# Kernel optimization log

Measured on AMD Instinct MI355X. Metric: run time of the kernel, lower is better.

## Reference

```python
import jax, jax.numpy as jnp
import numpy as np

EPS = 1e-6

def setup_inputs() -> dict:
    key = jax.random.key(0)
    ks = jax.random.split(key, 9)
    B, D, F = 8192, 2048, 1024
    s_in = 1.0 / np.sqrt(D)
    return {
        "Q": jax.random.normal(ks[0], (B, D), jnp.float32),
        "K": jax.random.normal(ks[1], (B, D), jnp.float32),
        "V": jax.random.normal(ks[2], (B, D), jnp.float32),
        "Wq": jax.random.normal(ks[3], (D, F), jnp.float32) * s_in,
        "bq": jnp.zeros((F,), jnp.float32),
        "Wk": jax.random.normal(ks[4], (D, F), jnp.float32) * s_in,
        "bk": jnp.zeros((F,), jnp.float32),
        "Wv": jax.random.normal(ks[5], (D, D), jnp.float32) * s_in,
        "bv": jnp.zeros((D,), jnp.float32),
    }

def reference(Q, K, V, Wq, bq, Wk, bk, Wv, bv):
    # feature maps: Linear + ELU (note: ELU, no +1, matching the source)
    Q_feat = jax.nn.elu(Q @ Wq + bq)          # (B, F)
    K_feat = jax.nn.elu(K @ Wk + bk)          # (B, F)
    V_proj = V @ Wv + bv                      # (B, D)
    # torch: KV = outer(K_feat, V_proj); QKV = Q_feat @ KV
    # equivalent without materializing (B, F, D):
    qk = jnp.einsum('bi,bi->b', Q_feat, K_feat)      # (B,)
    QKV = qk[:, None] * V_proj                        # (B, D)
    # Z = 1 / (sum_i Q_feat * sum_i K_feat + eps)
    Z = 1.0 / (Q_feat.sum(-1) * K_feat.sum(-1) + EPS)  # (B,)
    return QKV * Z[:, None]
```

## Files before the change

### kernel.cpp

```cpp
#include <hip/hip_runtime.h>
#include <hip/hip_fp16.h>
#include <cstdint>
#include <cstddef>

typedef _Float16 f16x8 __attribute__((ext_vector_type(8)));
typedef _Float16 f16x4 __attribute__((ext_vector_type(4)));
typedef float    f32x4 __attribute__((ext_vector_type(4)));

#define GPTR(p) ((const __attribute__((address_space(1))) void*)(p))
#define SPTR(p) ((__attribute__((address_space(3))) void*)(p))

__global__ void transpose_cast_kernel(const float* __restrict__ W,
                                      _Float16* __restrict__ Wt,
                                      int R, int C) {
  __shared__ float tile[32][33];
  const int c  = blockIdx.x * 32 + threadIdx.x;
  const int r0 = blockIdx.y * 32;
  for (int i = threadIdx.y; i < 32; i += 8)
    tile[i][threadIdx.x] = W[(size_t)(r0 + i) * C + c];
  __syncthreads();
  const int out_c = r0 + threadIdx.x;
  const int oc0   = blockIdx.x * 32;
  for (int i = threadIdx.y; i < 32; i += 8)
    Wt[(size_t)(oc0 + i) * R + out_c] = (_Float16)tile[threadIdx.x][i];
}

__global__ void cast_f32_f16_kernel(const float* __restrict__ src,
                                    _Float16* __restrict__ dst) {
  const size_t i = (size_t)blockIdx.x * 256 + threadIdx.x;
  const float4 v = ((const float4*)src)[i];
  f16x4 h;
  h[0] = (_Float16)v.x; h[1] = (_Float16)v.y;
  h[2] = (_Float16)v.z; h[3] = (_Float16)v.w;
  ((f16x4*)dst)[i] = h;
}

#define STG8(kk, h, slotv) do {                                                \
    __builtin_amdgcn_global_load_lds(GPTR(aRow + (h) * hstep + (kk)),          \
        SPTR(Aring + (slotv) * 4096 + wave * 512), 16, 0, 0);                  \
    __builtin_amdgcn_global_load_lds(GPTR(bRow + (h) * hstep + (kk)),          \
        SPTR(Bring + (slotv) * 4096 + wave * 512), 16, 0, 0);                  \
  } while (0)

#define WINDOW8(t_, DOSTG, VCSTR) do {                                         \
    const int e_ = (2 * (t_)) & 7;                                             \
    if (DOSTG) STG8(((t_) + 3) * 32, 0, (e_ + 6) & 7);                         \
    asm volatile("s_waitcnt vmcnt(" VCSTR ")" ::: "memory");                   \
    __builtin_amdgcn_s_barrier();                                              \
    asm volatile("" ::: "memory");                                             \
    const _Float16* Ab_ = Aring + ((e_ + wm) & 7) * 4096;                      \
    const _Float16* Bb_ = Bring + ((e_ + (wn >> 1)) & 7) * 4096               \
                          + (wn & 1) * 2048;                                   \
    f16x8 bf_[4], af_[4];                                                      \
    _Pragma("unroll")                                                          \
    for (int j_ = 0; j_ < 4; ++j_)                                             \
      bf_[j_] = *(const f16x8*)(Bb_ + j_ * 512 + lane_c * 8);                  \
    _Pragma("unroll")                                                          \
    for (int i_ = 0; i_ < 4; ++i_)                                             \
      af_[i_] = *(const f16x8*)(Ab_ + i_ * 512 + lane_c * 8);                  \
    __builtin_amdgcn_s_setprio(1);                                             \
    _Pragma("unroll")                                                          \
    for (int i_ = 0; i_ < 4; ++i_)                                             \
      _Pragma("unroll")                                                        \
      for (int j_ = 0; j_ < 4; ++j_)                                           \
        acc[i_][j_] = __builtin_amdgcn_mfma_f32_16x16x32_f16(af_[i_], bf_[j_], \
                                                             acc[i_][j_],      \
                                                             0, 0, 0);         \
    __builtin_amdgcn_s_setprio(0);                                             \
    asm volatile("" ::: "memory");                                             \
    __builtin_amdgcn_s_barrier();                                              \
    if (DOSTG) STG8(((t_) + 3) * 32, 1, (e_ + 7) & 7);                         \
    __builtin_amdgcn_s_barrier();                                              \
    asm volatile("" ::: "memory");                                             \
    _Pragma("unroll")                                                          \
    for (int i_ = 0; i_ < 4; ++i_)                                             \
      af_[i_] = *(const f16x8*)(Ab_ + (i_ + 4) * 512 + lane_c * 8);            \
    __builtin_amdgcn_s_setprio(1);                                             \
    _Pragma("unroll")                                                          \
    for (int i_ = 0; i_ < 4; ++i_)                                             \
      _Pragma("unroll")                                                        \
      for (int j_ = 0; j_ < 4; ++j_)                                           \
        acc[i_ + 4][j_] = __builtin_amdgcn_mfma_f32_16x16x32_f16(af_[i_],      \
                                                                 bf_[j_],      \
                                                                 acc[i_ + 4][j_],\
                                                                 0, 0, 0);     \
    __builtin_amdgcn_s_setprio(0);                                             \
    asm volatile("" ::: "memory");                                             \
    __builtin_amdgcn_s_barrier();                                              \
  } while (0)

template <int MODE, bool OUTHALF>
__global__ __launch_bounds__(512, 2) void gemm8p(
    const _Float16* __restrict__ A,
    const _Float16* __restrict__ Bt0, const _Float16* __restrict__ Bt1,
    const float* __restrict__ bias0, const float* __restrict__ bias1,
    int msplit, const float* __restrict__ scale,
    void* __restrict__ Cv, int K, int N) {
  __shared__ __align__(16) _Float16 Aring[8 * 4096];
  __shared__ __align__(16) _Float16 Bring[8 * 4096];

  const int tid  = threadIdx.x;
  const int lane = tid & 63;
  const int wave = tid >> 6;
  const int quad = lane >> 4;
  const int r    = lane & 15;
  const int wm   = wave >> 2;
  const int wn   = wave & 3;

  const int gx  = gridDim.x;
  const int nwg = gx * gridDim.y;
  int flat = blockIdx.y * gx + blockIdx.x;
  if ((nwg & 7) == 0) flat = (flat & 7) * (nwg >> 3) + (flat >> 3);
  const int m0 = (flat / gx) * 256;
  const int n0 = (flat % gx) * 256;

  const _Float16* Bt   = (m0 >= msplit) ? Bt1 : Bt0;
  const float*    bias = (m0 >= msplit) ? bias1 : bias0;

  const int sp  = tid >> 3;
  const int sub = (tid & 7) ^ (sp & 7);
  const int lr  = sp * 2 + (sub >> 2);
  const int sc  = sub & 3;
  const _Float16* aRow = A  + (size_t)(m0 + lr) * K + sc * 8;
  const _Float16* bRow = Bt + (size_t)(n0 + lr) * K + sc * 8;
  const int hstep = 128 * K;

  const int lane_c = (r >> 1) * 8 + (((((r & 1) << 2) | quad)) ^ (r >> 1));

  f32x4 acc[8][4] = {};
  const int NT = K >> 5;

#pragma unroll
  for (int tt = 0; tt < 3; ++tt) {
    STG8(tt * 32, 0, (2 * tt) & 7);
    STG8(tt * 32, 1, (2 * tt + 1) & 7);
  }

  for (int t = 0; t < NT - 3; ++t) WINDOW8(t, 1, "10");
  WINDOW8(NT - 3, 0, "8");
  WINDOW8(NT - 2, 0, "4");
  WINDOW8(NT - 1, 0, "0");

  float*    Cf = (float*)Cv;
  _Float16* Ch = (_Float16*)Cv;
#pragma unroll
  for (int i = 0; i < 8; ++i) {
    const int row0 = m0 + wm * 128 + i * 16 + quad * 4;
#pragma unroll
    for (int j = 0; j < 4; ++j) {
      const int col = n0 + wn * 64 + j * 16 + r;
      const float b = bias[col];
#pragma unroll
      for (int reg = 0; reg < 4; ++reg) {
        const int row = row0 + reg;
        float v = acc[i][j][reg] + b;
        if (MODE == 0) v = v > 0.f ? v : (expf(v) - 1.f);
        else           v = v * scale[row];
        if (OUTHALF) Ch[(size_t)row * N + col] = (_Float16)v;
        else         Cf[(size_t)row * N + col] = v;
      }
    }
  }
}

#undef STG8
#undef WINDOW8

template <int MODE, bool AHALF, bool OUTHALF>
__global__ __launch_bounds__(256) void gemm2(
    const void* __restrict__ Av,
    const _Float16* __restrict__ Bt0, const _Float16* __restrict__ Bt1,
    const float* __restrict__ bias0, const float* __restrict__ bias1,
    int msplit, const float* __restrict__ scale,
    void* __restrict__ Cv, int K, int N) {
  constexpr int BK = 64;
  __shared__ __align__(16) _Float16 As[128 * BK];
  __shared__ __align__(16) _Float16 Bs[128 * BK];

  const int tid  = threadIdx.x;
  const int lane = tid & 63;
  const int wave = tid >> 6;
  const int quad = lane >> 4;
  const int r    = lane & 15;
  const int wm   = wave >> 1;
  const int wn   = wave & 1;
  const int m0   = blockIdx.y * 128;
  const int n0   = blockIdx.x * 128;

  const _Float16* Bt  = (m0 >= msplit) ? Bt1 : Bt0;
  const float* bias   = (m0 >= msplit) ? bias1 : bias0;

  size_t aoff[4], boff[4];
  int slot[4];
#pragma unroll
  for (int t = 0; t < 4; ++t) {
    const int s  = wave * 256 + t * 64 + lane;
    const int n  = s >> 3;
    const int kc = (s & 7) ^ (n & 7);
    aoff[t] = (size_t)(m0 + n) * K + kc * 8;
    boff[t] = (size_t)(n0 + n) * K + kc * 8;
    slot[t] = s;
  }

  f32x4 acc[4][4] = {};
  const _Float16* Ah = (const _Float16*)Av;
  const float*    Af = (const float*)Av;

  for (int k0 = 0; k0 < K; k0 += BK) {
    __syncthreads();
    if (AHALF) {
#pragma unroll
      for (int t = 0; t < 4; ++t)
        __builtin_amdgcn_global_load_lds(GPTR(Ah + aoff[t] + k0),
                                         SPTR(As + (wave * 256 + t * 64) * 8),
                                         16, 0, 0);
    } else {
#pragma unroll
      for (int t = 0; t < 4; ++t) {
        const float* ap = Af + aoff[t] + k0;
        const float4 v0 = *(const float4*)ap;
        const float4 v1 = *(const float4*)(ap + 4);
        f16x8 h;
        h[0] = (_Float16)v0.x; h[1] = (_Float16)v0.y;
        h[2] = (_Float16)v0.z; h[3] = (_Float16)v0.w;
        h[4] = (_Float16)v1.x; h[5] = (_Float16)v1.y;
        h[6] = (_Float16)v1.z; h[7] = (_Float16)v1.w;
        *(f16x8*)(As + (size_t)slot[t] * 8) = h;
      }
    }
#pragma unroll
    for (int t = 0; t < 4; ++t)
      __builtin_amdgcn_global_load_lds(GPTR(Bt + boff[t] + k0),
                                       SPTR(Bs + (wave * 256 + t * 64) * 8),
                                       16, 0, 0);
    __syncthreads();

#pragma unroll
    for (int ki = 0; ki < 2; ++ki) {
      f16x8 af[4], bf[4];
#pragma unroll
      for (int i = 0; i < 4; ++i) {
        const int an = wm * 64 + i * 16 + r;
        af[i] = *(const f16x8*)(As + (an * 8 + ((ki * 4 + quad) ^ (an & 7))) * 8);
      }
#pragma unroll
      for (int j = 0; j < 4; ++j) {
        const int bn = wn * 64 + j * 16 + r;
        bf[j] = *(const f16x8*)(Bs + (bn * 8 + ((ki * 4 + quad) ^ (bn & 7))) * 8);
      }
#pragma unroll
      for (int i = 0; i < 4; ++i)
#pragma unroll
        for (int j = 0; j < 4; ++j)
          acc[i][j] = __builtin_amdgcn_mfma_f32_16x16x32_f16(af[i], bf[j],
                                                             acc[i][j], 0, 0, 0);
    }
  }

  float*    Cf = (float*)Cv;
  _Float16* Ch = (_Float16*)Cv;
#pragma unroll
  for (int i = 0; i < 4; ++i) {
#pragma unroll
    for (int j = 0; j < 4; ++j) {
      const int col = n0 + wn * 64 + j * 16 + r;
      const float b = bias[col];
#pragma unroll
      for (int reg = 0; reg < 4; ++reg) {
        const int row = m0 + wm * 64 + i * 16 + quad * 4 + reg;
        float v = acc[i][j][reg] + b;
        if (MODE == 0) v = v > 0.f ? v : (expf(v) - 1.f);
        else           v = v * scale[row];
        if (OUTHALF) Ch[(size_t)row * N + col] = (_Float16)v;
        else         Cf[(size_t)row * N + col] = v;
      }
    }
  }
}

template <bool HALF>
__global__ void reduce_scale2(const void* __restrict__ Qf,
                              const void* __restrict__ Kf,
                              float* __restrict__ scale) {
  const int b = blockIdx.x;
  const int t = threadIdx.x;
  float q[4], k[4];
  if (HALF) {
    const f16x4 qh = ((const f16x4*)((const _Float16*)Qf + (size_t)b * 1024))[t];
    const f16x4 kh = ((const f16x4*)((const _Float16*)Kf + (size_t)b * 1024))[t];
#pragma unroll
    for (int i = 0; i < 4; ++i) { q[i] = (float)qh[i]; k[i] = (float)kh[i]; }
  } else {
    const float4 qv = ((const float4*)((const float*)Qf + (size_t)b * 1024))[t];
    const float4 kv = ((const float4*)((const float*)Kf + (size_t)b * 1024))[t];
    q[0] = qv.x; q[1] = qv.y; q[2] = qv.z; q[3] = qv.w;
    k[0] = kv.x; k[1] = kv.y; k[2] = kv.z; k[3] = kv.w;
  }
  float qk = q[0] * k[0] + q[1] * k[1] + q[2] * k[2] + q[3] * k[3];
  float sq = q[0] + q[1] + q[2] + q[3];
  float sk = k[0] + k[1] + k[2] + k[3];
#pragma unroll
  for (int off = 32; off > 0; off >>= 1) {
    qk += __shfl_down(qk, off, 64);
    sq += __shfl_down(sq, off, 64);
    sk += __shfl_down(sk, off, 64);
  }
  __shared__ float buf[3][4];
  const int lane = t & 63, wv = t >> 6;
  if (lane == 0) { buf[0][wv] = qk; buf[1][wv] = sq; buf[2][wv] = sk; }
  __syncthreads();
  if (t == 0) {
    const float QK = buf[0][0] + buf[0][1] + buf[0][2] + buf[0][3];
    const float SQ = buf[1][0] + buf[1][1] + buf[1][2] + buf[1][3];
    const float SK = buf[2][0] + buf[2][1] + buf[2][2] + buf[2][3];
    scale[b] = QK / (SQ * SK + 1e-6f);
  }
}

extern "C" void kernel_launch(void* const* d_in, const int* in_sizes, int n_in,
                              void* d_out, int out_size, void* d_ws,
                              size_t ws_size, hipStream_t stream) {
  const float* Q  = (const float*)d_in[0];
  const float* K_ = (const float*)d_in[1];
  const float* V  = (const float*)d_in[2];
  const float* Wq = (const float*)d_in[3];
  const float* bq = (const float*)d_in[4];
  const float* Wk = (const float*)d_in[5];
  const float* bk = (const float*)d_in[6];
  const float* Wv = (const float*)d_in[7];
  const float* bv = (const float*)d_in[8];
  float* out = (float*)d_out;

  const int B = 8192, D = 2048, F = 1024;
  const size_t MiB = 1u << 20;
  char* ws = (char*)d_ws;

  const size_t NEED_FAST = 40 * MiB + 64 * 1024;

  if (ws_size >= NEED_FAST) {
    _Float16* WqT = (_Float16*)ws;
    _Float16* WkT = (_Float16*)(ws + 4 * MiB);
    _Float16* WvT = (_Float16*)ws;
    _Float16* QfH = (_Float16*)(ws + 8 * MiB);
    _Float16* KfH = (_Float16*)(ws + 24 * MiB);
    _Float16* Vh  = (_Float16*)(ws + 8 * MiB);
    float* scale  = (float*)(ws + 40 * MiB);
    _Float16* Qh = (_Float16*)d_out;
    _Float16* Kh = (_Float16*)d_out + (size_t)B * D;

    dim3 tb(32, 8);
    transpose_cast_kernel<<<dim3(F / 32, D / 32), tb, 0, stream>>>(Wq, WqT, D, F);
    transpose_cast_kernel<<<dim3(F / 32, D / 32), tb, 0, stream>>>(Wk, WkT, D, F);
    const int castBlocks = (B * D / 4) / 256;
    cast_f32_f16_kernel<<<castBlocks, 256, 0, stream>>>(Q,  Qh);
    cast_f32_f16_kernel<<<castBlocks, 256, 0, stream>>>(K_, Kh);

    gemm8p<0, true><<<dim3(F / 256, (2 * B) / 256), 512, 0, stream>>>(
        Qh, WqT, WkT, bq, bk, B, nullptr, QfH, D, F);
    reduce_scale2<true><<<B, 256, 0, stream>>>(QfH, KfH, scale);

    cast_f32_f16_kernel<<<castBlocks, 256, 0, stream>>>(V, Vh);
    transpose_cast_kernel<<<dim3(D / 32, D / 32), tb, 0, stream>>>(Wv, WvT, D, D);
    gemm8p<1, false><<<dim3(D / 256, B / 256), 512, 0, stream>>>(
        Vh, WvT, WvT, bv, bv, 1 << 30, scale, out, D, D);
  } else {
    _Float16* WqT = (_Float16*)ws;
    _Float16* WkT = (_Float16*)(ws + 4 * MiB);
    _Float16* WvT = (_Float16*)(ws + 8 * MiB);
    float* scale  = (float*)(ws + 16 * MiB);
    float* Qf = out;
    float* Kf = out + (size_t)B * F;

    dim3 tb(32, 8);
    transpose_cast_kernel<<<dim3(F / 32, D / 32), tb, 0, stream>>>(Wq, WqT, D, F);
    transpose_cast_kernel<<<dim3(F / 32, D / 32), tb, 0, stream>>>(Wk, WkT, D, F);
    transpose_cast_kernel<<<dim3(D / 32, D / 32), tb, 0, stream>>>(Wv, WvT, D, D);

    gemm2<0, false, false><<<dim3(F / 128, B / 128), 256, 0, stream>>>(
        Q, WqT, WqT, bq, bq, 1 << 30, nullptr, Qf, D, F);
    gemm2<0, false, false><<<dim3(F / 128, B / 128), 256, 0, stream>>>(
        K_, WkT, WkT, bk, bk, 1 << 30, nullptr, Kf, D, F);
    reduce_scale2<false><<<B, 256, 0, stream>>>(Qf, Kf, scale);
    gemm2<1, false, false><<<dim3(D / 128, B / 128), 256, 0, stream>>>(
        V, WvT, WvT, bv, bv, 1 << 30, scale, out, D, D);
  }
}
```

Baseline: 441.1 us.

## Collapse GEMM K-window to a single barrier and issue prefetch mid-MFMA

```diff
diff --git a/kernel.cpp b/kernel.cpp
--- a/kernel.cpp
+++ b/kernel.cpp
@@ -42,51 +42,45 @@
         SPTR(Bring + (slotv) * 4096 + wave * 512), 16, 0, 0);                  \
   } while (0)
 
-#define WINDOW8(t_, DOSTG, VCSTR) do {                                         \
+#define WINDOW8(t_, DOSTG, DOWAIT, VCSTR) do {                                 \
     const int e_ = (2 * (t_)) & 7;                                             \
-    if (DOSTG) STG8(((t_) + 3) * 32, 0, (e_ + 6) & 7);                         \
-    asm volatile("s_waitcnt vmcnt(" VCSTR ")" ::: "memory");                   \
-    __builtin_amdgcn_s_barrier();                                              \
-    asm volatile("" ::: "memory");                                             \
     const _Float16* Ab_ = Aring + ((e_ + wm) & 7) * 4096;                      \
-    const _Float16* Bb_ = Bring + ((e_ + (wn >> 1)) & 7) * 4096               \
+    const _Float16* Bb_ = Bring + ((e_ + (wn >> 1)) & 7) * 4096                \
                           + (wn & 1) * 2048;                                   \
-    f16x8 bf_[4], af_[4];                                                      \
+    f16x8 bf_[4], afL_[4], afH_[4];                                            \
     _Pragma("unroll")                                                          \
     for (int j_ = 0; j_ < 4; ++j_)                                             \
       bf_[j_] = *(const f16x8*)(Bb_ + j_ * 512 + lane_c * 8);                  \
     _Pragma("unroll")                                                          \
     for (int i_ = 0; i_ < 4; ++i_)                                             \
-      af_[i_] = *(const f16x8*)(Ab_ + i_ * 512 + lane_c * 8);                  \
+      afL_[i_] = *(const f16x8*)(Ab_ + i_ * 512 + lane_c * 8);                 \
+    _Pragma("unroll")                                                          \
+    for (int i_ = 0; i_ < 4; ++i_)                                             \
+      afH_[i_] = *(const f16x8*)(Ab_ + (i_ + 4) * 512 + lane_c * 8);           \
     __builtin_amdgcn_s_setprio(1);                                             \
     _Pragma("unroll")                                                          \
     for (int i_ = 0; i_ < 4; ++i_)                                             \
       _Pragma("unroll")                                                        \
       for (int j_ = 0; j_ < 4; ++j_)                                           \
-        acc[i_][j_] = __builtin_amdgcn_mfma_f32_16x16x32_f16(af_[i_], bf_[j_], \
+        acc[i_][j_] = __builtin_amdgcn_mfma_f32_16x16x32_f16(afL_[i_], bf_[j_],\
                                                              acc[i_][j_],      \
                                                              0, 0, 0);         \
-    __builtin_amdgcn_s_setprio(0);                                             \
-    asm volatile("" ::: "memory");                                             \
-    __builtin_amdgcn_s_barrier();                                              \
-    if (DOSTG) STG8(((t_) + 3) * 32, 1, (e_ + 7) & 7);                         \
-    __builtin_amdgcn_s_barrier();                                              \
-    asm volatile("" ::: "memory");                                             \
-    _Pragma("unroll")                                                          \
-    for (int i_ = 0; i_ < 4; ++i_)                                             \
-      af_[i_] = *(const f16x8*)(Ab_ + (i_ + 4) * 512 + lane_c * 8);            \
-    __builtin_amdgcn_s_setprio(1);                                             \
+    if (DOSTG) {                                                               \
+      STG8(((t_) + 3) * 32, 0, (e_ + 6) & 7);                                  \
+      STG8(((t_) + 3) * 32, 1, (e_ + 7) & 7);                                  \
+    }                                                                          \
     _Pragma("unroll")                                                          \
     for (int i_ = 0; i_ < 4; ++i_)                                             \
       _Pragma("unroll")                                                        \
       for (int j_ = 0; j_ < 4; ++j_)                                           \
-        acc[i_ + 4][j_] = __builtin_amdgcn_mfma_f32_16x16x32_f16(af_[i_],      \
+        acc[i_ + 4][j_] = __builtin_amdgcn_mfma_f32_16x16x32_f16(afH_[i_],     \
                                                                  bf_[j_],      \
                                                                  acc[i_ + 4][j_],\
                                                                  0, 0, 0);     \
     __builtin_amdgcn_s_setprio(0);                                             \
+    if (DOWAIT) asm volatile("s_waitcnt vmcnt(" VCSTR ")" ::: "memory");       \
+    __builtin_amdgcn_s_barrier();                                              \
     asm volatile("" ::: "memory");                                             \
-    __builtin_amdgcn_s_barrier();                                              \
   } while (0)
 
 template <int MODE, bool OUTHALF>
@@ -135,11 +129,14 @@
     STG8(tt * 32, 0, (2 * tt) & 7);
     STG8(tt * 32, 1, (2 * tt + 1) & 7);
   }
-
-  for (int t = 0; t < NT - 3; ++t) WINDOW8(t, 1, "10");
-  WINDOW8(NT - 3, 0, "8");
-  WINDOW8(NT - 2, 0, "4");
-  WINDOW8(NT - 1, 0, "0");
+  asm volatile("s_waitcnt vmcnt(8)" ::: "memory");
+  __builtin_amdgcn_s_barrier();
+  asm volatile("" ::: "memory");
+
+  for (int t = 0; t < NT - 3; ++t) WINDOW8(t, 1, 1, "8");
+  WINDOW8(NT - 3, 0, 1, "4");
+  WINDOW8(NT - 2, 0, 1, "0");
+  WINDOW8(NT - 1, 0, 0, "0");
 
   float*    Cf = (float*)Cv;
   _Float16* Ch = (_Float16*)Cv;
```

New measurement: 394.5 us. 10.5% less time.
